# Optimization experiments

Hardware: AMD Instinct MI355X
Metric: run time of the kernel (lower is better)

## Reference

```python
import jax, jax.numpy as jnp
import numpy as np

# cfg constants (match init_kwargs)
K_CFG = 32
SPOT_K = 16
K_NN = max(K_CFG + 1, SPOT_K)  # = 33
DOWN_K = 8
SIGMA_C = 3.0
SEED_NUM = 128
SEED_THRESHOLD = 0.5

B, N, M, NC, MC = 1, 4096, 4096, 512, 512
CF, CC, H = 256, 1024, 256


def pairwise_sqdist(x, y):
    # x:(B,n,3) y:(B,m,3) -> (B,n,m) squared euclidean distance
    xx = jnp.sum(x * x, -1, keepdims=True)          # (B,n,1)
    yy = jnp.sum(y * y, -1, keepdims=True)          # (B,m,1)
    return xx - 2.0 * jnp.einsum('bnd,bmd->bnm', x, y) + jnp.swapaxes(yy, 1, 2)


def knn_idx(d, k):
    # smallest-k indices along last dim
    return jax.lax.top_k(-d, k)[1]


def compatibility(ref_d, src_d, mi):
    # ref_d:(B,N,N) src_d:(B,M,M) mi:(B,N) int -> (B,N) mean compatibility
    g = jnp.take_along_axis(src_d, mi[:, :, None], axis=1)   # (B,N,M) rows gathered
    g = jnp.take_along_axis(g, mi[:, None, :], axis=2)       # (B,N,N) cols gathered
    return jnp.mean(jax.nn.relu(1.0 - jnp.abs(ref_d - g) / SIGMA_C), axis=-1)


def seeding(compat, conf):
    # faithful to torch: selection = compat < max(compat)*threshold, weighted by confidence
    # jit-friendly fixed-size topk (seed_num) instead of data-dependent max_num
    sel = (compat < compat.max(-1, keepdims=True) * SEED_THRESHOLD).astype(conf.dtype)
    return jax.lax.top_k(sel * conf, SEED_NUM)[1]            # (B,SEED_NUM)


def setup_inputs() -> dict:
    key = jax.random.key(0)
    ks = jax.random.split(key, 12)
    inp = {
        'ref_points': jax.random.normal(ks[0], (B, N, 3), jnp.float32),
        'src_points': jax.random.normal(ks[1], (B, M, 3), jnp.float32),
        'ref_feats': jax.random.normal(ks[2], (B, N, CF), jnp.float32),
        'src_feats': jax.random.normal(ks[3], (B, M, CF), jnp.float32),
        'ref_points_c': jax.random.normal(ks[4], (B, NC, 3), jnp.float32),
        'src_points_c': jax.random.normal(ks[5], (B, MC, 3), jnp.float32),
        'ref_feats_c': jax.random.normal(ks[6], (B, NC, CC), jnp.float32),
        'src_feats_c': jax.random.normal(ks[7], (B, MC, CC), jnp.float32),
        'W1': jax.random.normal(ks[8], (CC, H), jnp.float32) / np.sqrt(CC),
        'b1': jnp.zeros((H,), jnp.float32),
        'W2': jax.random.normal(ks[9], (CF, H), jnp.float32) / np.sqrt(CF),
        'b2': jnp.zeros((H,), jnp.float32),
    }
    return inp


def reference(ref_points, src_points, ref_feats, src_feats,
              ref_points_c, src_points_c, ref_feats_c, src_feats_c,
              W1, b1, W2, b2):
    # --- KNN neighbor search (torch.no_grad block) ---
    ref_dists = pairwise_sqdist(ref_points, ref_points)     # (B,N,N)
    src_dists = pairwise_sqdist(src_points, src_points)     # (B,M,M)
    ref_idx = knn_idx(ref_dists, K_NN)                      # (B,N,K_NN)
    src_idx = knn_idx(src_dists, K_NN)
    ref_idx_up = knn_idx(pairwise_sqdist(ref_points, ref_points_c), 1)[..., 0]   # (B,N)
    src_idx_up = knn_idx(pairwise_sqdist(src_points, src_points_c), 1)[..., 0]
    ref_idx_down = knn_idx(pairwise_sqdist(ref_points_c, ref_points), DOWN_K)    # (B,NC,DOWN_K)
    src_idx_down = knn_idx(pairwise_sqdist(src_points_c, src_points), DOWN_K)

    # --- input projections ---
    hf_ref = ref_feats @ W2 + b2                            # (B,N,H)
    hf_src = src_feats @ W2 + b2
    hc_ref = ref_feats_c @ W1 + b1                          # (B,NC,H)
    hc_src = src_feats_c @ W1 + b1

    # --- dual-softmax matching scores ---
    scores = jnp.einsum('bnc,bmc->bnm', hf_ref, hf_src)     # (B,N,M)
    scores = jax.nn.softmax(scores, axis=-1) * jax.nn.softmax(scores, axis=-2)

    # --- ref -> src direction ---
    conf_r = jnp.max(scores, axis=-1)                       # (B,N)
    mi_r = jnp.argmax(scores, axis=-1)                      # (B,N)
    compat_r = compatibility(ref_dists, src_dists, mi_r)    # (B,N)
    seed_r = seeding(compat_r, conf_r * compat_r)           # (B,SEED_NUM)
    spot_r = jnp.take_along_axis(src_idx[..., :SPOT_K], mi_r[:, :, None], axis=1)  # (B,N,SPOT_K)

    # --- src -> ref direction ---
    scores_t = jnp.swapaxes(scores, 1, 2)
    conf_s = jnp.max(scores_t, axis=-1)
    mi_s = jnp.argmax(scores_t, axis=-1)
    compat_s = compatibility(src_dists, ref_dists, mi_s)
    seed_s = seeding(compat_s, conf_s * compat_s)
    spot_s = jnp.take_along_axis(ref_idx[..., :SPOT_K], mi_s[:, :, None], axis=1)

    return (scores, compat_r, compat_s, seed_r, seed_s, spot_r, spot_s,
            hc_ref, hc_src, ref_idx_up, src_idx_up, ref_idx_down, src_idx_down)
```

## Files before the change

### kernel.cpp

```cpp
#include <hip/hip_runtime.h>
#include <math.h>

#define NP 4096
#define NCP 512
#define HD 256
#define CCD 1024
#define SPOTK 16
#define DOWNK 8
#define SEEDN 128
#define JCH 512
#define NJC (NP / JCH)

__global__ __launch_bounds__(256) void gemm128_bt(
    const float* __restrict__ A, const float* __restrict__ B,
    float* __restrict__ C,
    float* __restrict__ pmaxR, float* __restrict__ psumR,
    float* __restrict__ pmaxC, float* __restrict__ psumC,
    int M, int N, int K)
{
    const int PAD = 132;
    __shared__ float As[32 * 132];
    __shared__ float Bs[32 * 132];

    const int bm = blockIdx.y * 128, bn = blockIdx.x * 128;
    const int t = threadIdx.x;
    const int tx = t & 15, ty = t >> 4;

    float acc[2][2][4][4] = {};

    for (int k0 = 0; k0 < K; k0 += 32) {
#pragma unroll
        for (int it = 0; it < 4; it++) {
            int idx = t + it * 256;
            int row = idx >> 3, kc = (idx & 7) * 4;
            float4 va = *(const float4*)&A[(size_t)(bm + row) * K + k0 + kc];
            As[(kc + 0) * PAD + row] = va.x;
            As[(kc + 1) * PAD + row] = va.y;
            As[(kc + 2) * PAD + row] = va.z;
            As[(kc + 3) * PAD + row] = va.w;
            float4 vb = *(const float4*)&B[(size_t)(bn + row) * K + k0 + kc];
            Bs[(kc + 0) * PAD + row] = vb.x;
            Bs[(kc + 1) * PAD + row] = vb.y;
            Bs[(kc + 2) * PAD + row] = vb.z;
            Bs[(kc + 3) * PAD + row] = vb.w;
        }
        __syncthreads();
#pragma unroll
        for (int kk = 0; kk < 32; kk++) {
            float4 a0 = *(const float4*)&As[kk * PAD + ty * 4];
            float4 a1 = *(const float4*)&As[kk * PAD + ty * 4 + 64];
            float4 b0 = *(const float4*)&Bs[kk * PAD + tx * 4];
            float4 b1 = *(const float4*)&Bs[kk * PAD + tx * 4 + 64];
            float ar[2][4] = {{a0.x, a0.y, a0.z, a0.w}, {a1.x, a1.y, a1.z, a1.w}};
            float br[2][4] = {{b0.x, b0.y, b0.z, b0.w}, {b1.x, b1.y, b1.z, b1.w}};
#pragma unroll
            for (int qr = 0; qr < 2; qr++)
#pragma unroll
                for (int qc = 0; qc < 2; qc++)
#pragma unroll
                    for (int i = 0; i < 4; i++)
#pragma unroll
                        for (int j = 0; j < 4; j++)
                            acc[qr][qc][i][j] = fmaf(ar[qr][i], br[qc][j], acc[qr][qc][i][j]);
        }
        __syncthreads();
    }

#pragma unroll
    for (int qr = 0; qr < 2; qr++)
#pragma unroll
        for (int i = 0; i < 4; i++) {
            int m = bm + qr * 64 + ty * 4 + i;
#pragma unroll
            for (int qc = 0; qc < 2; qc++) {
                int n = bn + qc * 64 + tx * 4;
                float4 v = make_float4(acc[qr][qc][i][0], acc[qr][qc][i][1],
                                       acc[qr][qc][i][2], acc[qr][qc][i][3]);
                *(float4*)&C[(size_t)m * N + n] = v;
            }
        }

#pragma unroll
    for (int qr = 0; qr < 2; qr++)
#pragma unroll
        for (int i = 0; i < 4; i++) {
            float m = -INFINITY;
#pragma unroll
            for (int qc = 0; qc < 2; qc++)
#pragma unroll
                for (int j = 0; j < 4; j++) m = fmaxf(m, acc[qr][qc][i][j]);
            float s = 0.f;
#pragma unroll
            for (int qc = 0; qc < 2; qc++)
#pragma unroll
                for (int j = 0; j < 4; j++) s += expf(acc[qr][qc][i][j] - m);
#pragma unroll
            for (int off = 1; off < 16; off <<= 1) {
                float om = __shfl_xor(m, off), os = __shfl_xor(s, off);
                float Mx = fmaxf(m, om);
                s = s * expf(m - Mx) + os * expf(om - Mx);
                m = Mx;
            }
            if (tx == 0) {
                int r = bm + qr * 64 + ty * 4 + i;
                pmaxR[(size_t)blockIdx.x * NP + r] = m;
                psumR[(size_t)blockIdx.x * NP + r] = s;
            }
        }

    float* colm = As;
    float* cols_ = Bs;
#pragma unroll
    for (int qc = 0; qc < 2; qc++)
#pragma unroll
        for (int j = 0; j < 4; j++) {
            float m = -INFINITY;
#pragma unroll
            for (int qr = 0; qr < 2; qr++)
#pragma unroll
                for (int i = 0; i < 4; i++) m = fmaxf(m, acc[qr][qc][i][j]);
            float s = 0.f;
#pragma unroll
            for (int qr = 0; qr < 2; qr++)
#pragma unroll
                for (int i = 0; i < 4; i++) s += expf(acc[qr][qc][i][j] - m);
#pragma unroll
            for (int off = 16; off < 64; off <<= 1) {
                float om = __shfl_xor(m, off), os = __shfl_xor(s, off);
                float Mx = fmaxf(m, om);
                s = s * expf(m - Mx) + os * expf(om - Mx);
                m = Mx;
            }
            if ((ty & 3) == 0) {
                int w = ty >> 2, c = qc * 64 + tx * 4 + j;
                colm[w * 132 + c] = m;
                cols_[w * 132 + c] = s;
            }
        }
    __syncthreads();
    if (t < 128) {
        int c = t;
        float m = colm[c], s = cols_[c];
#pragma unroll
        for (int w = 1; w < 4; w++) {
            float om = colm[w * 132 + c], os = cols_[w * 132 + c];
            float Mx = fmaxf(m, om);
            s = s * expf(m - Mx) + os * expf(om - Mx);
            m = Mx;
        }
        pmaxC[(size_t)blockIdx.y * NP + bn + c] = m;
        psumC[(size_t)blockIdx.y * NP + bn + c] = s;
    }
}

__global__ __launch_bounds__(256) void combine_stats(
    const float* __restrict__ pmaxA, const float* __restrict__ psumA,
    const float* __restrict__ pmaxB, const float* __restrict__ psumB,
    float* omaxA, float* osumA, float* omaxB, float* osumB)
{
    const float* pmax = blockIdx.z ? pmaxB : pmaxA;
    const float* psum = blockIdx.z ? psumB : psumA;
    float* omax       = blockIdx.z ? omaxB : omaxA;
    float* osum       = blockIdx.z ? osumB : osumA;
    int m = blockIdx.x * 256 + threadIdx.x;
    float mx = -INFINITY;
    for (int c = 0; c < 32; c++) mx = fmaxf(mx, pmax[(size_t)c * NP + m]);
    float sum = 0.f;
    for (int c = 0; c < 32; c++) sum += psum[(size_t)c * NP + m] * expf(pmax[(size_t)c * NP + m] - mx);
    omax[m] = mx; osum[m] = sum;
}

__global__ __launch_bounds__(256) void gemm64(
    const float* __restrict__ A0, const float* __restrict__ A1,
    const float* __restrict__ B, const float* __restrict__ bias,
    float* __restrict__ C0, float* __restrict__ C1,
    int M, int N, int K)
{
    const float* A = blockIdx.z ? A1 : A0;
    float* C = blockIdx.z ? C1 : C0;

    const int PAD = 68;
    __shared__ float As[16 * 68];
    __shared__ float Bs[16 * 68];

    const int bm = blockIdx.y * 64, bn = blockIdx.x * 64;
    const int t = threadIdx.x;
    const int tx = t & 15, ty = t >> 4;

    float acc[4][4] = {};

    for (int k0 = 0; k0 < K; k0 += 16) {
        {
            int row = t >> 2, kc = (t & 3) * 4;
            float4 v = *(const float4*)&A[(size_t)(bm + row) * K + k0 + kc];
            As[(kc + 0) * PAD + row] = v.x;
            As[(kc + 1) * PAD + row] = v.y;
            As[(kc + 2) * PAD + row] = v.z;
            As[(kc + 3) * PAD + row] = v.w;
        }
        {
            int k = t >> 4, n4 = (t & 15) * 4;
            float4 v = *(const float4*)&B[(size_t)(k0 + k) * N + bn + n4];
            *(float4*)&Bs[k * PAD + n4] = v;
        }
        __syncthreads();
#pragma unroll
        for (int kk = 0; kk < 16; kk++) {
            float4 a4 = *(const float4*)&As[kk * PAD + ty * 4];
            float4 b4 = *(const float4*)&Bs[kk * PAD + tx * 4];
            float ar[4] = {a4.x, a4.y, a4.z, a4.w};
            float br[4] = {b4.x, b4.y, b4.z, b4.w};
#pragma unroll
            for (int i = 0; i < 4; i++)
#pragma unroll
                for (int j = 0; j < 4; j++)
                    acc[i][j] = fmaf(ar[i], br[j], acc[i][j]);
        }
        __syncthreads();
    }
    float4 b4 = *(const float4*)&bias[bn + tx * 4];
#pragma unroll
    for (int i = 0; i < 4; i++) {
        int m = bm + ty * 4 + i;
        float4 v = make_float4(acc[i][0] + b4.x, acc[i][1] + b4.y,
                               acc[i][2] + b4.z, acc[i][3] + b4.w);
        *(float4*)&C[(size_t)m * N + bn + tx * 4] = v;
    }
}

__global__ __launch_bounds__(256) void gemm64_atomic(
    const float* __restrict__ A0, const float* __restrict__ A1,
    const float* __restrict__ B,
    float* __restrict__ C0, float* __restrict__ C1,
    int M, int N, int K, int KCH)
{
    int pair = blockIdx.z >> 3, ks = blockIdx.z & 7;
    const float* A = pair ? A1 : A0;
    float* C = pair ? C1 : C0;

    const int PAD = 68;
    __shared__ float As[16 * 68];
    __shared__ float Bs[16 * 68];

    const int bm = blockIdx.y * 64, bn = blockIdx.x * 64;
    const int t = threadIdx.x;
    const int tx = t & 15, ty = t >> 4;
    const int kbeg = ks * KCH, kend = kbeg + KCH;

    float acc[4][4] = {};

    for (int k0 = kbeg; k0 < kend; k0 += 16) {
        {
            int row = t >> 2, kc = (t & 3) * 4;
            float4 v = *(const float4*)&A[(size_t)(bm + row) * K + k0 + kc];
            As[(kc + 0) * PAD + row] = v.x;
            As[(kc + 1) * PAD + row] = v.y;
            As[(kc + 2) * PAD + row] = v.z;
            As[(kc + 3) * PAD + row] = v.w;
        }
        {
            int k = t >> 4, n4 = (t & 15) * 4;
            float4 v = *(const float4*)&B[(size_t)(k0 + k) * N + bn + n4];
            *(float4*)&Bs[k * PAD + n4] = v;
        }
        __syncthreads();
#pragma unroll
        for (int kk = 0; kk < 16; kk++) {
            float4 a4 = *(const float4*)&As[kk * PAD + ty * 4];
            float4 b4 = *(const float4*)&Bs[kk * PAD + tx * 4];
            float ar[4] = {a4.x, a4.y, a4.z, a4.w};
            float br[4] = {b4.x, b4.y, b4.z, b4.w};
#pragma unroll
            for (int i = 0; i < 4; i++)
#pragma unroll
                for (int j = 0; j < 4; j++)
                    acc[i][j] = fmaf(ar[i], br[j], acc[i][j]);
        }
        __syncthreads();
    }
#pragma unroll
    for (int i = 0; i < 4; i++) {
        int m = bm + ty * 4 + i;
#pragma unroll
        for (int j = 0; j < 4; j++)
            atomicAdd(&C[(size_t)m * N + bn + tx * 4 + j], acc[i][j]);
    }
}

__global__ void init_hc(const float* __restrict__ b1,
                        float* __restrict__ o_hcr, float* __restrict__ o_hcs)
{
    int idx = blockIdx.x * 256 + threadIdx.x;
    float b = b1[idx & (HD - 1)];
    o_hcr[idx] = b; o_hcs[idx] = b;
}

__global__ void pack_pts(const float* __restrict__ p0, const float* __restrict__ p1,
                         const float* __restrict__ p2, const float* __restrict__ p3,
                         float4* o0, float4* o1, float4* o2, float4* o3)
{
    int z = blockIdx.z;
    const float* p = (z == 0) ? p0 : (z == 1) ? p1 : (z == 2) ? p2 : p3;
    float4* o      = (z == 0) ? o0 : (z == 1) ? o1 : (z == 2) ? o2 : o3;
    int n = (z < 2) ? NP : NCP;
    int i = blockIdx.x * 256 + threadIdx.x;
    if (i >= n) return;
    float x = p[i * 3], y = p[i * 3 + 1], zz = p[i * 3 + 2];
    o[i] = make_float4(x, y, zz, x * x + y * y + zz * zz);
}

__global__ __launch_bounds__(256) void finalize_rows(float* __restrict__ s,
    const float* __restrict__ rmax, const float* __restrict__ rsum,
    const float* __restrict__ cmax, const float* __restrict__ csum,
    float* __restrict__ confr, int* __restrict__ mir)
{
    int n = blockIdx.x;
    float rm = rmax[n], rs = rsum[n];
    size_t base = (size_t)n * NP;
    float best = -INFINITY; int bi = 0x7fffffff;
    for (int m1 = threadIdx.x; m1 < NP; m1 += 256) {
        float v = s[base + m1];
        float a = expf(v - rm) / rs;
        float b = expf(v - cmax[m1]) / csum[m1];
        float sc = a * b;
        s[base + m1] = sc;
        if (sc > best) { best = sc; bi = m1; }
    }
    __shared__ float rv[256]; __shared__ int ri[256];
    rv[threadIdx.x] = best; ri[threadIdx.x] = bi; __syncthreads();
    for (int off = 128; off; off >>= 1) {
        if (threadIdx.x < off) {
            float v2 = rv[threadIdx.x + off]; int i2 = ri[threadIdx.x + off];
            if (v2 > rv[threadIdx.x] || (v2 == rv[threadIdx.x] && i2 < ri[threadIdx.x])) {
                rv[threadIdx.x] = v2; ri[threadIdx.x] = i2;
            }
        }
        __syncthreads();
    }
    if (threadIdx.x == 0) { confr[n] = rv[0]; mir[n] = ri[0]; }
}

__global__ __launch_bounds__(256) void col_argmax_partial(const float* __restrict__ s,
                                                          float* pconf, int* pmi)
{
    int m = blockIdx.x * 256 + threadIdx.x;
    int n0 = blockIdx.y * 128;
    float best = -INFINITY; int bi = 0;
    for (int n = n0; n < n0 + 128; n++) {
        float v = s[(size_t)n * NP + m];
        if (v > best) { best = v; bi = n; }
    }
    pconf[(size_t)blockIdx.y * NP + m] = best;
    pmi[(size_t)blockIdx.y * NP + m] = bi;
}

__global__ __launch_bounds__(256) void col_argmax_combine(const float* __restrict__ pconf,
                                                          const int* __restrict__ pmi,
                                                          float* confs, int* mis)
{
    int m = blockIdx.x * 256 + threadIdx.x;
    float best = -INFINITY; int bi = 0;
    for (int c = 0; c < 32; c++) {
        float v = pconf[(size_t)c * NP + m];
        if (v > best) { best = v; bi = pmi[(size_t)c * NP + m]; }
    }
    confs[m] = best; mis[m] = bi;
}

__global__ void gather_spot(
    const float4* __restrict__ sp4, const float4* __restrict__ rp4,
    const int* __restrict__ sidx16, const int* __restrict__ ridx16,
    const int* __restrict__ mir, const int* __restrict__ mis,
    float4* __restrict__ qr, float4* __restrict__ qs,
    float* __restrict__ o_spotr, float* __restrict__ o_spots)
{
    int z = blockIdx.z;
    int t = blockIdx.x * 256 + threadIdx.x;
    if (z < 2) {
        if (t >= NP) return;
        const float4* p4 = z ? rp4 : sp4;
        const int*    mi = z ? mis : mir;
        float4*       q  = z ? qs : qr;
        q[t] = p4[mi[t]];
    } else {
        int n = t >> 4, k = t & 15;
        const int* idx16 = (z == 2) ? sidx16 : ridx16;
        const int* mi    = (z == 2) ? mir : mis;
        float* outp      = (z == 2) ? o_spotr : o_spots;
        outp[t] = (float)idx16[(size_t)mi[n] * SPOTK + k];
    }
}

__global__ __launch_bounds__(256) void compat_kernel(
    const float4* __restrict__ baseA, const float4* __restrict__ baseB,
    const float4* __restrict__ qA, const float4* __restrict__ qB,
    float* __restrict__ o1A, float* __restrict__ o1B,
    float* __restrict__ o2A, float* __restrict__ o2B)
{
    const float4* base = blockIdx.z ? baseB : baseA;
    const float4* q    = blockIdx.z ? qB : qA;
    float* out1        = blockIdx.z ? o1B : o1A;
    float* out2        = blockIdx.z ? o2B : o2A;
    int n = blockIdx.x;
    float4 b = base[n];
    float4 a = q[n];
    float sum = 0.f;
    for (int j = threadIdx.x; j < NP; j += 256) {
        float4 p = base[j];
        float rt = b.x * p.x + b.y * p.y + b.z * p.z;
        float rd = (b.w - 2.f * rt) + p.w;
        float4 qj = q[j];
        float st = a.x * qj.x + a.y * qj.y + a.z * qj.z;
        float sd = (a.w - 2.f * st) + qj.w;
        float c = 1.f - fabsf(rd - sd) / 3.0f;
        sum += fmaxf(c, 0.f);
    }
    __shared__ float red[256];
    red[threadIdx.x] = sum; __syncthreads();
    for (int off = 128; off; off >>= 1) {
        if (threadIdx.x < off) red[threadIdx.x] += red[threadIdx.x + off];
        __syncthreads();
    }
    if (threadIdx.x == 0) { float c = red[0] * (1.0f / NP); out1[n] = c; out2[n] = c; }
}

__global__ __launch_bounds__(256) void seed_prep(
    const float* __restrict__ compatA, const float* __restrict__ compatB,
    const float* __restrict__ confA, const float* __restrict__ confB,
    float* __restrict__ wA, float* __restrict__ wB)
{
    const float* compat = blockIdx.z ? compatB : compatA;
    const float* conf   = blockIdx.z ? confB : confA;
    float* w            = blockIdx.z ? wB : wA;
    __shared__ float red[256];
    int tid = threadIdx.x;
    float mx = -INFINITY;
    for (int j = tid; j < NP; j += 256) mx = fmaxf(mx, compat[j]);
    red[tid] = mx; __syncthreads();
    for (int off = 128; off; off >>= 1) {
        if (tid < off) red[tid] = fmaxf(red[tid], red[tid + off]);
        __syncthreads();
    }
    float thr = red[0] * 0.5f;
    for (int j = tid; j < NP; j += 256) {
        float c = compat[j];
        w[j] = (c < thr) ? conf[j] * c : 0.0f;
    }
}

__global__ __launch_bounds__(256) void seed_rank_partial(
    const float* __restrict__ wA, const float* __restrict__ wB,
    int* __restrict__ rankpA, int* __restrict__ rankpB)
{
    const float* w = blockIdx.z ? wB : wA;
    int* rankp     = blockIdx.z ? rankpB : rankpA;
    int tid = threadIdx.x;
    int jc = blockIdx.y;

    __shared__ float4 wj[JCH / 4];
    if (tid < JCH / 4) wj[tid] = ((const float4*)w)[jc * (JCH / 4) + tid];
    __syncthreads();

    int i = blockIdx.x * 256 + tid;
    float wi = w[i];
    int jbase = jc * JCH;
    int r0 = 0, r1 = 0, r2 = 0, r3 = 0;
#pragma unroll 4
    for (int j4 = 0; j4 < JCH / 4; j4++) {
        float4 v = wj[j4];
        int j = jbase + j4 * 4;
        r0 += (v.x > wi || (v.x == wi && (j    ) < i));
        r1 += (v.y > wi || (v.y == wi && (j + 1) < i));
        r2 += (v.z > wi || (v.z == wi && (j + 2) < i));
        r3 += (v.w > wi || (v.w == wi && (j + 3) < i));
    }
    rankp[(size_t)jc * NP + i] = (r0 + r1) + (r2 + r3);
}

__global__ __launch_bounds__(256) void seed_scatter(
    const int* __restrict__ rankpA, const int* __restrict__ rankpB,
    float* __restrict__ outA, float* __restrict__ outB)
{
    const int* rankp = blockIdx.z ? rankpB : rankpA;
    float* outp      = blockIdx.z ? outB : outA;
    int i = blockIdx.x * 256 + threadIdx.x;
    int r = 0;
#pragma unroll
    for (int jc = 0; jc < NJC; jc++) r += rankp[(size_t)jc * NP + i];
    if (r < SEEDN) outp[r] = (float)i;
}

__device__ __forceinline__ void bitonic64_val(float& d, int lane)
{
#pragma unroll
    for (int k = 2; k <= 64; k <<= 1)
#pragma unroll
        for (int j = k >> 1; j > 0; j >>= 1) {
            float od = __shfl_xor(d, j);
            bool lower = ((lane & j) == 0);
            bool asc   = ((lane & k) == 0);
            bool take = (lower == asc) ? (od < d) : (d < od);
            d = take ? od : d;
        }
}

__device__ __forceinline__ void bitonic64_lex(float& d, int& i, int lane)
{
#pragma unroll
    for (int k = 2; k <= 64; k <<= 1)
#pragma unroll
        for (int j = k >> 1; j > 0; j >>= 1) {
            float od = __shfl_xor(d, j);
            int   oi = __shfl_xor(i, j);
            bool lower = ((lane & j) == 0);
            bool asc   = ((lane & k) == 0);
            bool less = (od < d) || (od == d && oi < i);
            bool gtr  = (d < od) || (d == od && i < oi);
            bool take = (lower == asc) ? less : gtr;
            d = take ? od : d;
            i = take ? oi : i;
        }
}

template<int KSEL>
__device__ __forceinline__ void merge_chunk(float& run_d, int& run_i,
                                            float cd, int ci, int lane)
{
    bitonic64_lex(cd, ci, lane);
    int src = lane - KSEL;
    int s2 = (src >= 0 && src < KSEL) ? src : 0;
    float cd2 = __shfl(cd, s2);
    int   ci2 = __shfl(ci, s2);
    float nd = (lane < KSEL) ? run_d : ((lane < 2 * KSEL) ? cd2 : INFINITY);
    int   ni = (lane < KSEL) ? run_i : ((lane < 2 * KSEL) ? ci2 : 0x7fffffff);
    bitonic64_lex(nd, ni, lane);
    run_d = nd; run_i = ni;
}

template<int KSEL>
__global__ __launch_bounds__(256) void knn_topk(
    const float4* __restrict__ rowA, const float4* __restrict__ rowB,
    const float4* __restrict__ colA, const float4* __restrict__ colB,
    int ncols,
    int* __restrict__ outiA, int* __restrict__ outiB,
    float* __restrict__ outfA, float* __restrict__ outfB)
{
    const float4* rowp = blockIdx.z ? rowB : rowA;
    const float4* colp = blockIdx.z ? colB : colA;
    int* outi = blockIdx.z ? outiB : outiA;
    float* outf = blockIdx.z ? outfB : outfA;

    int wid = threadIdx.x >> 6, lane = threadIdx.x & 63;
    int r = blockIdx.x * 4 + wid;

    float4 p = rowp[r];

    float mn = INFINITY;
    for (int j0 = 0; j0 < ncols; j0 += 64) {
        float4 c = colp[j0 + lane];
        float t = p.x * c.x + p.y * c.y + p.z * c.z;
        float d = (p.w - 2.f * t) + c.w;
        mn = fminf(mn, d);
    }
    bitonic64_val(mn, lane);
    float T = __shfl(mn, KSEL - 1) + 1e-4f;

    __shared__ float qd[4][256];
    __shared__ int   qi[4][256];
    int cnt = 0; bool ovf = false;
    for (int j0 = 0; j0 < ncols; j0 += 64) {
        int j = j0 + lane;
        float4 c = colp[j];
        float t = p.x * c.x + p.y * c.y + p.z * c.z;
        float d = (p.w - 2.f * t) + c.w;
        bool keep = (d <= T);
        unsigned long long mask = __ballot(keep);
        int nsel = __popcll(mask);
        if (cnt + nsel > 256) { ovf = true; break; }
        if (keep) {
            int pos = cnt + (int)__popcll(mask & ((1ull << lane) - 1ull));
            qd[wid][pos] = d; qi[wid][pos] = j;
        }
        cnt += nsel;
    }

    float run_d = INFINITY; int run_i = 0x7fffffff;
    if (!ovf) {
        for (int c = 0; c < cnt; c += 64) {
            int idx = c + lane;
            float cd = (idx < cnt) ? qd[wid][idx] : INFINITY;
            int   ci = (idx < cnt) ? qi[wid][idx] : 0x7fffffff;
            merge_chunk<KSEL>(run_d, run_i, cd, ci, lane);
        }
    } else {
        for (int j0 = 0; j0 < ncols; j0 += 64) {
            int j = j0 + lane;
            float4 c = colp[j];
            float t = p.x * c.x + p.y * c.y + p.z * c.z;
            float d = (p.w - 2.f * t) + c.w;
            merge_chunk<KSEL>(run_d, run_i, d, j, lane);
        }
    }

    if (lane < KSEL) {
        if (outi) outi[(size_t)r * KSEL + lane] = run_i;
        else      outf[(size_t)r * KSEL + lane] = (float)run_i;
    }
}

__global__ __launch_bounds__(256) void up_argmin(
    const float4* __restrict__ ptsA, const float4* __restrict__ ptsB,
    const float4* __restrict__ ptscA, const float4* __restrict__ ptscB,
    float* __restrict__ outA, float* __restrict__ outB)
{
    const float4* pts   = blockIdx.z ? ptsB : ptsA;
    const float4* pts_c = blockIdx.z ? ptscB : ptscA;
    float* out_f        = blockIdx.z ? outB : outA;
    __shared__ float4 cp[NCP];
    for (int c = threadIdx.x; c < NCP; c += 256) cp[c] = pts_c[c];
    __syncthreads();
    int n = blockIdx.x * 256 + threadIdx.x;
    float4 p = pts[n];
    float best = INFINITY; int bi = 0;
    for (int c = 0; c < NCP; c++) {
        float4 q = cp[c];
        float t = p.x * q.x + p.y * q.y + p.z * q.z;
        float d = (p.w - 2.f * t) + q.w;
        if (d < best) { best = d; bi = c; }
    }
    out_f[n] = (float)bi;
}

extern "C" void kernel_launch(void* const* d_in, const int* in_sizes, int n_in,
                              void* d_out, int out_size, void* d_ws, size_t ws_size,
                              hipStream_t stream)
{
    const float* ref_points   = (const float*)d_in[0];
    const float* src_points   = (const float*)d_in[1];
    const float* ref_feats    = (const float*)d_in[2];
    const float* src_feats    = (const float*)d_in[3];
    const float* ref_points_c = (const float*)d_in[4];
    const float* src_points_c = (const float*)d_in[5];
    const float* ref_feats_c  = (const float*)d_in[6];
    const float* src_feats_c  = (const float*)d_in[7];
    const float* W1 = (const float*)d_in[8];
    const float* b1 = (const float*)d_in[9];
    const float* W2 = (const float*)d_in[10];
    const float* b2 = (const float*)d_in[11];

    float* out = (float*)d_out;
    float* o_scores = out;
    float* o_compr  = o_scores + (size_t)NP * NP;
    float* o_comps  = o_compr + NP;
    float* o_seedr  = o_comps + NP;
    float* o_seeds  = o_seedr + SEEDN;
    float* o_spotr  = o_seeds + SEEDN;
    float* o_spots  = o_spotr + (size_t)NP * SPOTK;
    float* o_hcr    = o_spots + (size_t)NP * SPOTK;
    float* o_hcs    = o_hcr + (size_t)NCP * HD;
    float* o_rup    = o_hcs + (size_t)NCP * HD;
    float* o_sup    = o_rup + NP;
    float* o_rdown  = o_sup + NP;
    float* o_sdown  = o_rdown + (size_t)NCP * DOWNK;

    float* ws = (float*)d_ws;
    float* hfr   = ws;
    float* hfs   = hfr + (size_t)NP * HD;
    float* rmax  = hfs + (size_t)NP * HD;
    float* rsum  = rmax + NP;
    float* cmax  = rsum + NP;
    float* csum  = cmax + NP;
    float* confr = csum + NP;
    float* confs = confr + NP;
    float* compr = confs + NP;
    float* comps = compr + NP;
    int*   mir   = (int*)(comps + NP);
    int*   mis   = mir + NP;
    float* pmax  = (float*)(mis + NP);
    float* psum  = pmax + 32 * NP;
    float* pconf = psum + 32 * NP;
    int*   pmi   = (int*)(pconf + 32 * NP);
    float4* qr   = (float4*)(pmi + 32 * NP);
    float4* qs   = qr + NP;
    int* ridx16  = (int*)(qs + NP);
    int* sidx16  = ridx16 + (size_t)NP * SPOTK;
    float4* rp4  = (float4*)(sidx16 + (size_t)NP * SPOTK);
    float4* sp4  = rp4 + NP;
    float4* rcp4 = sp4 + NP;
    float4* scp4 = rcp4 + NCP;
    float* wA    = (float*)(scp4 + NCP);
    float* wB    = wA + NP;
    int* rankpA  = (int*)(wB + NP);
    int* rankpB  = rankpA + NJC * NP;
    size_t ws_need = (size_t)((float*)(rankpB + NJC * NP) - ws) * 4;
    if (ws_size < ws_need) return;

    float* pmaxR = pconf;
    float* psumR = (float*)pmi;

    dim3 b256(256);

    pack_pts<<<dim3(NP / 256, 1, 4), b256, 0, stream>>>(
        ref_points, src_points, ref_points_c, src_points_c, rp4, sp4, rcp4, scp4);

    init_hc<<<dim3((NCP * HD) / 256), b256, 0, stream>>>(b1, o_hcr, o_hcs);
    gemm64_atomic<<<dim3(HD / 64, NCP / 64, 16), b256, 0, stream>>>(
        ref_feats_c, src_feats_c, W1, o_hcr, o_hcs, NCP, HD, CCD, CCD / 8);

    gemm64<<<dim3(HD / 64, NP / 64, 2), b256, 0, stream>>>(
        ref_feats, src_feats, W2, b2, hfr, hfs, NP, HD, HD);

    gemm128_bt<<<dim3(32, 32, 1), b256, 0, stream>>>(
        hfr, hfs, o_scores, pmaxR, psumR, pmax, psum, NP, NP, HD);
    combine_stats<<<dim3(16, 1, 2), b256, 0, stream>>>(
        pmaxR, psumR, pmax, psum, rmax, rsum, cmax, csum);

    knn_topk<SPOTK><<<dim3(NP / 4, 1, 2), b256, 0, stream>>>(
        rp4, sp4, rp4, sp4, NP, ridx16, sidx16, nullptr, nullptr);
    knn_topk<DOWNK><<<dim3(NCP / 4, 1, 2), b256, 0, stream>>>(
        rcp4, scp4, rp4, sp4, NP, nullptr, nullptr, o_rdown, o_sdown);
    up_argmin<<<dim3(NP / 256, 1, 2), b256, 0, stream>>>(
        rp4, sp4, rcp4, scp4, o_rup, o_sup);

    finalize_rows<<<NP, b256, 0, stream>>>(o_scores, rmax, rsum, cmax, csum, confr, mir);
    col_argmax_partial<<<dim3(16, 32), b256, 0, stream>>>(o_scores, pconf, pmi);
    col_argmax_combine<<<16, b256, 0, stream>>>(pconf, pmi, confs, mis);

    gather_spot<<<dim3((NP * SPOTK) / 256, 1, 4), b256, 0, stream>>>(
        sp4, rp4, sidx16, ridx16, mir, mis, qr, qs, o_spotr, o_spots);

    compat_kernel<<<dim3(NP, 1, 2), b256, 0, stream>>>(
        rp4, sp4, qr, qs, o_compr, o_comps, compr, comps);

    seed_prep<<<dim3(1, 1, 2), b256, 0, stream>>>(
        compr, comps, confr, confs, wA, wB);
    seed_rank_partial<<<dim3(NP / 256, NJC, 2), b256, 0, stream>>>(
        wA, wB, rankpA, rankpB);
    seed_scatter<<<dim3(NP / 256, 1, 2), b256, 0, stream>>>(
        rankpA, rankpB, o_seedr, o_seeds);
}
```

Before: 516.9 us.

## Fuse score finalization with row and column argmax; merge bias init into pack

Replaces the per-row finalize kernel plus the separate two-pass column argmax with one tiled kernel. Each block handles 64 rows by 1024 columns, writes the dual-softmax product once, and produces partial row and column maxima, which a small combine kernel then reduces. This removes a second full read of the 4096x4096 score matrix and one launch. The bias-init kernel is folded into pack_pts as extra z-slices. The tradeoff is a block-wide __syncthreads per row and only 256 blocks, which may limit occupancy and latency hiding.

```diff
diff --git a/kernel.cpp b/kernel.cpp
--- a/kernel.cpp
+++ b/kernel.cpp
@@ -287,19 +287,19 @@
     }
 }
 
-__global__ void init_hc(const float* __restrict__ b1,
-                        float* __restrict__ o_hcr, float* __restrict__ o_hcs)
-{
-    int idx = blockIdx.x * 256 + threadIdx.x;
-    float b = b1[idx & (HD - 1)];
-    o_hcr[idx] = b; o_hcs[idx] = b;
-}
-
 __global__ void pack_pts(const float* __restrict__ p0, const float* __restrict__ p1,
                          const float* __restrict__ p2, const float* __restrict__ p3,
-                         float4* o0, float4* o1, float4* o2, float4* o3)
+                         const float* __restrict__ b1,
+                         float4* o0, float4* o1, float4* o2, float4* o3,
+                         float* __restrict__ o_hcr, float* __restrict__ o_hcs)
 {
     int z = blockIdx.z;
+    if (z >= 4) {
+        float* o = (z == 4) ? o_hcr : o_hcs;
+        for (int idx = blockIdx.x * 256 + threadIdx.x; idx < NCP * HD; idx += 16 * 256)
+            o[idx] = b1[idx & (HD - 1)];
+        return;
+    }
     const float* p = (z == 0) ? p0 : (z == 1) ? p1 : (z == 2) ? p2 : p3;
     float4* o      = (z == 0) ? o0 : (z == 1) ? o1 : (z == 2) ? o2 : o3;
     int n = (z < 2) ? NP : NCP;
@@ -309,62 +309,95 @@
     o[i] = make_float4(x, y, zz, x * x + y * y + zz * zz);
 }
 
-__global__ __launch_bounds__(256) void finalize_rows(float* __restrict__ s,
+__global__ __launch_bounds__(256) void finalize_fused(
+    float* __restrict__ s,
     const float* __restrict__ rmax, const float* __restrict__ rsum,
     const float* __restrict__ cmax, const float* __restrict__ csum,
-    float* __restrict__ confr, int* __restrict__ mir)
-{
-    int n = blockIdx.x;
-    float rm = rmax[n], rs = rsum[n];
-    size_t base = (size_t)n * NP;
-    float best = -INFINITY; int bi = 0x7fffffff;
-    for (int m1 = threadIdx.x; m1 < NP; m1 += 256) {
-        float v = s[base + m1];
-        float a = expf(v - rm) / rs;
-        float b = expf(v - cmax[m1]) / csum[m1];
-        float sc = a * b;
-        s[base + m1] = sc;
-        if (sc > best) { best = sc; bi = m1; }
-    }
-    __shared__ float rv[256]; __shared__ int ri[256];
-    rv[threadIdx.x] = best; ri[threadIdx.x] = bi; __syncthreads();
-    for (int off = 128; off; off >>= 1) {
-        if (threadIdx.x < off) {
-            float v2 = rv[threadIdx.x + off]; int i2 = ri[threadIdx.x + off];
-            if (v2 > rv[threadIdx.x] || (v2 == rv[threadIdx.x] && i2 < ri[threadIdx.x])) {
-                rv[threadIdx.x] = v2; ri[threadIdx.x] = i2;
+    float* __restrict__ rowpV, int* __restrict__ rowpI,
+    float* __restrict__ colV, int* __restrict__ colI)
+{
+    int tid = threadIdx.x;
+    int bc = blockIdx.x;
+    int br = blockIdx.y;
+    int c = bc * 1024 + tid * 4;
+    int lane = tid & 63, wid = tid >> 6;
+
+    float4 cm4 = *(const float4*)&cmax[c];
+    float4 cs4 = *(const float4*)&csum[c];
+    float cv[4] = {-INFINITY, -INFINITY, -INFINITY, -INFINITY};
+    int   ci[4] = {0, 0, 0, 0};
+
+    __shared__ float rv[4]; __shared__ int ri[4];
+
+    for (int r = 0; r < 64; r++) {
+        int row = br * 64 + r;
+        float rm = rmax[row], rs = rsum[row];
+        float4 v = *(const float4*)&s[(size_t)row * NP + c];
+        float sc[4];
+        {
+            float a0 = expf(v.x - rm) / rs, b0 = expf(v.x - cm4.x) / cs4.x; sc[0] = a0 * b0;
+            float a1 = expf(v.y - rm) / rs, b1_ = expf(v.y - cm4.y) / cs4.y; sc[1] = a1 * b1_;
+            float a2 = expf(v.z - rm) / rs, b2_ = expf(v.z - cm4.z) / cs4.z; sc[2] = a2 * b2_;
+            float a3 = expf(v.w - rm) / rs, b3_ = expf(v.w - cm4.w) / cs4.w; sc[3] = a3 * b3_;
+        }
+        *(float4*)&s[(size_t)row * NP + c] = make_float4(sc[0], sc[1], sc[2], sc[3]);
+
+#pragma unroll
+        for (int j = 0; j < 4; j++)
+            if (sc[j] > cv[j]) { cv[j] = sc[j]; ci[j] = row; }
+
+        float bv = sc[0]; int bi = c;
+#pragma unroll
+        for (int j = 1; j < 4; j++)
+            if (sc[j] > bv) { bv = sc[j]; bi = c + j; }
+#pragma unroll
+        for (int off = 1; off < 64; off <<= 1) {
+            float ov = __shfl_xor(bv, off); int oi = __shfl_xor(bi, off);
+            if (ov > bv || (ov == bv && oi < bi)) { bv = ov; bi = oi; }
+        }
+        if (lane == 0) { rv[wid] = bv; ri[wid] = bi; }
+        __syncthreads();
+        if (tid == 0) {
+            float gv = rv[0]; int gi = ri[0];
+#pragma unroll
+            for (int w = 1; w < 4; w++) {
+                float ov = rv[w]; int oi = ri[w];
+                if (ov > gv || (ov == gv && oi < gi)) { gv = ov; gi = oi; }
             }
-        }
-        __syncthreads();
-    }
-    if (threadIdx.x == 0) { confr[n] = rv[0]; mir[n] = ri[0]; }
-}
-
-__global__ __launch_bounds__(256) void col_argmax_partial(const float* __restrict__ s,
-                                                          float* pconf, int* pmi)
-{
-    int m = blockIdx.x * 256 + threadIdx.x;
-    int n0 = blockIdx.y * 128;
-    float best = -INFINITY; int bi = 0;
-    for (int n = n0; n < n0 + 128; n++) {
-        float v = s[(size_t)n * NP + m];
-        if (v > best) { best = v; bi = n; }
-    }
-    pconf[(size_t)blockIdx.y * NP + m] = best;
-    pmi[(size_t)blockIdx.y * NP + m] = bi;
-}
-
-__global__ __launch_bounds__(256) void col_argmax_combine(const float* __restrict__ pconf,
-                                                          const int* __restrict__ pmi,
-                                                          float* confs, int* mis)
-{
-    int m = blockIdx.x * 256 + threadIdx.x;
-    float best = -INFINITY; int bi = 0;
-    for (int c = 0; c < 32; c++) {
-        float v = pconf[(size_t)c * NP + m];
-        if (v > best) { best = v; bi = pmi[(size_t)c * NP + m]; }
-    }
-    confs[m] = best; mis[m] = bi;
+            rowpV[(size_t)bc * NP + row] = gv;
+            rowpI[(size_t)bc * NP + row] = gi;
+        }
+        __syncthreads();
+    }
+
+    *(float4*)&colV[(size_t)br * NP + c] = make_float4(cv[0], cv[1], cv[2], cv[3]);
+    *(int4*)&colI[(size_t)br * NP + c]   = make_int4(ci[0], ci[1], ci[2], ci[3]);
+}
+
+__global__ __launch_bounds__(256) void argmax_combine(
+    const float* __restrict__ rowpV, const int* __restrict__ rowpI,
+    const float* __restrict__ colV, const int* __restrict__ colI,
+    float* __restrict__ confr, int* __restrict__ mir,
+    float* __restrict__ confs, int* __restrict__ mis)
+{
+    int i = blockIdx.x * 256 + threadIdx.x;
+    if (blockIdx.z == 0) {
+        float best = -INFINITY; int bi = 0x7fffffff;
+#pragma unroll
+        for (int ch = 0; ch < 4; ch++) {
+            float v = rowpV[(size_t)ch * NP + i];
+            int  ix = rowpI[(size_t)ch * NP + i];
+            if (v > best || (v == best && ix < bi)) { best = v; bi = ix; }
+        }
+        confr[i] = best; mir[i] = bi;
+    } else {
+        float best = -INFINITY; int bi = 0;
+        for (int ch = 0; ch < 64; ch++) {
+            float v = colV[(size_t)ch * NP + i];
+            if (v > best) { best = v; bi = colI[(size_t)ch * NP + i]; }
+        }
+        confs[i] = best; mis[i] = bi;
+    }
 }
 
 __global__ void gather_spot(
@@ -692,18 +725,22 @@
     float* wB    = wA + NP;
     int* rankpA  = (int*)(wB + NP);
     int* rankpB  = rankpA + NJC * NP;
-    size_t ws_need = (size_t)((float*)(rankpB + NJC * NP) - ws) * 4;
+    float* rowpV = (float*)(rankpB + NJC * NP);
+    int*   rowpI = (int*)(rowpV + 4 * NP);
+    size_t ws_need = (size_t)((float*)(rowpI + 4 * NP) - ws) * 4;
     if (ws_size < ws_need) return;
 
     float* pmaxR = pconf;
     float* psumR = (float*)pmi;
+    float* colV  = pmax;
+    int*   colI  = (int*)pconf;
 
     dim3 b256(256);
 
-    pack_pts<<<dim3(NP / 256, 1, 4), b256, 0, stream>>>(
-        ref_points, src_points, ref_points_c, src_points_c, rp4, sp4, rcp4, scp4);
-
-    init_hc<<<dim3((NCP * HD) / 256), b256, 0, stream>>>(b1, o_hcr, o_hcs);
+    pack_pts<<<dim3(NP / 256, 1, 6), b256, 0, stream>>>(
+        ref_points, src_points, ref_points_c, src_points_c, b1,
+        rp4, sp4, rcp4, scp4, o_hcr, o_hcs);
+
     gemm64_atomic<<<dim3(HD / 64, NCP / 64, 16), b256, 0, stream>>>(
         ref_feats_c, src_feats_c, W1, o_hcr, o_hcs, NCP, HD, CCD, CCD / 8);
 
@@ -722,9 +759,10 @@
     up_argmin<<<dim3(NP / 256, 1, 2), b256, 0, stream>>>(
         rp4, sp4, rcp4, scp4, o_rup, o_sup);
 
-    finalize_rows<<<NP, b256, 0, stream>>>(o_scores, rmax, rsum, cmax, csum, confr, mir);
-    col_argmax_partial<<<dim3(16, 32), b256, 0, stream>>>(o_scores, pconf, pmi);
-    col_argmax_combine<<<16, b256, 0, stream>>>(pconf, pmi, confs, mis);
+    finalize_fused<<<dim3(4, 64), b256, 0, stream>>>(
+        o_scores, rmax, rsum, cmax, csum, rowpV, rowpI, colV, colI);
+    argmax_combine<<<dim3(16, 1, 2), b256, 0, stream>>>(
+        rowpV, rowpI, colV, colI, confr, mir, confs, mis);
 
     gather_spot<<<dim3((NP * SPOTK) / 256, 1, 4), b256, 0, stream>>>(
         sp4, rp4, sidx16, ridx16, mir, mis, qr, qs, o_spotr, o_spots);
```

New measurement: 596.7 us. 15.4% more time.
